# Kernel optimization log

Hardware: AMD Instinct MI355X
Metric: run time of the kernel (lower is better)

Reference implementation:

```python
import jax, jax.numpy as jnp
import numpy as np

N_NODES = 100000
NUM_FEATURES = 64
HIDDEN = 128
OUT_CONV2 = 100


def gcn_conv(x, W, b, src, dst, n):
    """PyG GCNConv: add self-loops, symmetric degree norm, scatter-add."""
    x = x @ W  # [N, out]
    loop = jnp.arange(n, dtype=src.dtype)
    src2 = jnp.concatenate([src, loop])  # [E+N]
    dst2 = jnp.concatenate([dst, loop])
    deg = jax.ops.segment_sum(jnp.ones_like(dst2, dtype=x.dtype), dst2, num_segments=n)
    dinv = jnp.where(deg > 0, deg ** -0.5, 0.0)
    norm = dinv[src2] * dinv[dst2]  # [E+N]
    msg = x[src2] * norm[:, None]  # gather + scale
    out = jax.ops.segment_sum(msg, dst2, num_segments=n)  # scatter-add
    return out + b


def setup_inputs() -> dict:
    key = jax.random.key(0)
    ks = jax.random.split(key, 8)
    E = 1600000
    x = jax.random.normal(ks[0], (N_NODES, NUM_FEATURES), dtype=jnp.float32)
    edge_index = jax.random.randint(ks[1], (2, E), 0, N_NODES, dtype=jnp.int64)
    # Glorot-style init for GCNConv weights, zeros bias (PyG defaults)
    s1 = (6.0 / (NUM_FEATURES + HIDDEN)) ** 0.5
    W1 = jax.random.uniform(ks[2], (NUM_FEATURES, HIDDEN), minval=-s1, maxval=s1, dtype=jnp.float32)
    b1 = jnp.zeros((HIDDEN,), dtype=jnp.float32)
    s2 = (6.0 / (HIDDEN + OUT_CONV2)) ** 0.5
    W2 = jax.random.uniform(ks[3], (HIDDEN, OUT_CONV2), minval=-s2, maxval=s2, dtype=jnp.float32)
    b2 = jnp.zeros((OUT_CONV2,), dtype=jnp.float32)
    sl = (1.0 / OUT_CONV2) ** 0.5
    Wl = jax.random.uniform(ks[4], (OUT_CONV2, 1), minval=-sl, maxval=sl, dtype=jnp.float32)
    bl = jax.random.uniform(ks[5], (1,), minval=-sl, maxval=sl, dtype=jnp.float32)
    return {"x": x, "edge_index": edge_index, "W1": W1, "b1": b1,
            "W2": W2, "b2": b2, "Wl": Wl, "bl": bl}


def reference(x, edge_index, W1, b1, W2, b2, Wl, bl):
    src, dst = edge_index[0], edge_index[1]
    h = gcn_conv(x, W1, b1, src, dst, N_NODES)
    h = jax.nn.relu(h)
    # F.dropout with training=False (eval/inference) is identity
    h = gcn_conv(h, W2, b2, src, dst, N_NODES)
    return h @ Wl + bl  # [N, 1]
```

## Files before the change

kernel.cpp:

```cpp
#include <hip/hip_runtime.h>
#include <hip/hip_fp16.h>


#define N_NODES 100000
#define F_IN 64
#define HID 128
#define OUT2 100
#define BSHIFT 7
#define BNODES 128
#define NBUCKETS ((N_NODES + BNODES - 1) / BNODES)
#define SCAP 2560
#define ACHUNK 4096
#define NB_PAD 1024
#define SENTB 0xFFFFu
#define SENTE 0xFFFFFFFFu
#define TSHIFT 13
#define NTILES 13
#define RSTRIDE 76
#define YSCALE 4096.0f
#define YINV   (1.0f / 4096.0f)
#define ZSCALE 8192.0f
#define ZINV   (1.0f / 8192.0f)

typedef _Float16 half8 __attribute__((ext_vector_type(8)));
typedef float f32x4 __attribute__((ext_vector_type(4)));

static __device__ __forceinline__ half8 as_half8(uint4 u) {
    union { uint4 u; half8 h; } x; x.u = u; return x.h;
}

__global__ __launch_bounds__(256) void prep_kernel(
    const float* __restrict__ W1, const float* __restrict__ W2,
    const float* __restrict__ b2, const float* __restrict__ Wl,
    const float* __restrict__ bl,
    float* __restrict__ v, float* __restrict__ c, uint4* __restrict__ Wpk,
    int* __restrict__ bcur) {
    int t = threadIdx.x;
    if (blockIdx.x < 8) {
        int idx = blockIdx.x * 256 + t;
        int lane2 = idx & 63;
        int kf    = (idx >> 6) & 1;
        int cb    = (idx >> 7) & 7;
        int part  = (idx >> 10) & 1;
        union { uint4 u; unsigned short s[8]; } pk;
        #pragma unroll
        for (int j = 0; j < 8; ++j) {
            int k    = kf * 32 + (lane2 >> 4) * 8 + j;
            int colg = cb * 16 + (lane2 & 15);
            float w = W1[k * HID + colg];
            __half h = __float2half_rn(w);
            if (part) h = __float2half_rn(w - __half2float(h));
            pk.s[j] = __half_as_ushort(h);
        }
        Wpk[idx] = pk.u;
    } else {
        #pragma unroll
        for (int i = 0; i < 4; ++i) bcur[t + i * 256] = (t + i * 256) * SCAP;
        if (t < HID) {
            float acc = 0.f;
            for (int k = 0; k < OUT2; ++k) acc += W2[t * OUT2 + k] * Wl[k];
            v[t] = acc;
        } else if (t == HID) {
            float acc = bl[0];
            for (int k = 0; k < OUT2; ++k) acc += b2[k] * Wl[k];
            *c = acc;
        }
    }
}

__global__ __launch_bounds__(256) void partA_kernel(
    const int* __restrict__ src, const int* __restrict__ dst,
    int* __restrict__ bcur, unsigned int* __restrict__ ebuf, int E) {
    __shared__ unsigned int stage[ACHUNK];
    __shared__ unsigned short sb[ACHUNK];
    __shared__ int hist[NB_PAD];
    __shared__ int ocnt[NB_PAD];
    __shared__ int gbase[NB_PAD];
    __shared__ int cnt2[NB_PAD];
    int t = threadIdx.x;
    int base = blockIdx.x * ACHUNK;
    int total = E - base; if (total > ACHUNK) total = ACHUNK;

    #pragma unroll
    for (int i = 0; i < 4; ++i) { hist[t + i * 256] = 0; cnt2[t + i * 256] = 0; }
    __syncthreads();

    unsigned int pe[16];
    unsigned short bk[16];
    #pragma unroll
    for (int k = 0; k < 16; ++k) {
        int e = base + k * 256 + t;
        if (e < E) {
            int s = src[e], d = dst[e];
            pe[k] = ((unsigned int)s << BSHIFT) | (unsigned int)(d & (BNODES - 1));
            bk[k] = (unsigned short)(d >> BSHIFT);
            atomicAdd(&hist[bk[k]], 1);
        } else {
            bk[k] = SENTB;
        }
    }
    __syncthreads();
    #pragma unroll
    for (int i = 0; i < 4; ++i) ocnt[t + i * 256] = hist[t + i * 256];
    __syncthreads();
    for (int off = 1; off < NB_PAD; off <<= 1) {
        int v4[4];
        #pragma unroll
        for (int i = 0; i < 4; ++i) {
            int p = t + i * 256;
            v4[i] = (p >= off) ? hist[p - off] : 0;
        }
        __syncthreads();
        #pragma unroll
        for (int i = 0; i < 4; ++i) hist[t + i * 256] += v4[i];
        __syncthreads();
    }
    #pragma unroll
    for (int i = 0; i < 4; ++i) {
        int b = (t + i * 256 + blockIdx.x * 131) & (NB_PAD - 1);
        int cc = ocnt[b];
        if (cc > 0 && b < NBUCKETS) gbase[b] = atomicAdd(&bcur[b], cc);
    }
    __syncthreads();
    #pragma unroll
    for (int k = 0; k < 16; ++k) {
        if (bk[k] != SENTB) {
            int b = bk[k];
            int pos = (hist[b] - ocnt[b]) + atomicAdd(&cnt2[b], 1);
            stage[pos] = pe[k];
            sb[pos] = (unsigned short)b;
        }
    }
    __syncthreads();
    #pragma unroll
    for (int k = 0; k < 16; ++k) {
        int idx = k * 256 + t;
        if (idx < total) {
            int b = sb[idx];
            int lo = hist[b] - ocnt[b];
            ebuf[gbase[b] + (idx - lo)] = stage[idx];
        }
    }
}

__global__ __launch_bounds__(256) void partB_kernel(
    const int* __restrict__ bcur, unsigned int* __restrict__ csr,
    float* __restrict__ dinv,
    const float4* __restrict__ x4, uint2* __restrict__ y2, int n) {
    __shared__ int lcnt[BNODES];
    __shared__ float sdinv[BNODES];
    __shared__ int tcnt[16];
    __shared__ int tcur[16];
    __shared__ unsigned int sbuf[SCAP];
    int b = blockIdx.x, t = threadIdx.x;
    int node0 = b << BSHIFT;
    int nlocal = min(BNODES, n - node0);
    int base = b * SCAP;
    int cnt = bcur[b] - base;
    if (t < BNODES) lcnt[t] = 0;
    if (t < 16) tcnt[t] = 0;
    __syncthreads();
    unsigned int er[SCAP / 256];
    #pragma unroll
    for (int k = 0; k < SCAP / 256; ++k) {
        int idx = k * 256 + t;
        er[k] = (idx < cnt) ? csr[base + idx] : SENTE;
        if (er[k] != SENTE) {
            atomicAdd(&lcnt[er[k] & (BNODES - 1)], 1);
            atomicAdd(&tcnt[er[k] >> (BSHIFT + TSHIFT)], 1);
        }
    }
    __syncthreads();
    if (t < BNODES) {
        float sd = rsqrtf((float)lcnt[t] + 1.0f);
        sdinv[t] = sd;
        if (t < nlocal) dinv[node0 + t] = sd;
    }
    if (t == 0) {
        int s = 0;
        #pragma unroll
        for (int i = 0; i < NTILES; ++i) { tcur[i] = s; s += tcnt[i]; }
    }
    __syncthreads();
    #pragma unroll
    for (int k = 0; k < SCAP / 256; ++k) {
        unsigned int e = er[k];
        if (e != SENTE) {
            int p = atomicAdd(&tcur[e >> (BSHIFT + TSHIFT)], 1);
            sbuf[p] = e;
        }
    }
    __syncthreads();
    for (int idx = t; idx < cnt; idx += 256) csr[base + idx] = sbuf[idx];
    for (int i = t; i < nlocal * 16; i += 256) {
        int nl = i >> 4;
        int gi = (node0 + nl) * 16 + (i & 15);
        float sc = sdinv[nl] * YSCALE;
        float4 xv = x4[gi];
        int a0 = __float2int_rn(xv.x * sc);
        int a1 = __float2int_rn(xv.y * sc);
        int a2 = __float2int_rn(xv.z * sc);
        int a3 = __float2int_rn(xv.w * sc);
        uint2 pk;
        pk.x = ((unsigned int)a0 & 0xFFFFu) | ((unsigned int)a1 << 16);
        pk.y = ((unsigned int)a2 & 0xFFFFu) | ((unsigned int)a3 << 16);
        y2[gi] = pk;
    }
}

__global__ __launch_bounds__(256, 4) void fused1_kernel(
    const int4* __restrict__ y4, const short* __restrict__ yh,
    const unsigned int* __restrict__ csr, const int* __restrict__ bcur,
    const float* __restrict__ dinv, const uint4* __restrict__ Wpk,
    const float* __restrict__ b1, const float* __restrict__ v,
    float* __restrict__ zz, int n) {
    __shared__ int acci[BNODES * RSTRIDE];
    int t = threadIdx.x;
    int lane = t & 63, wave = t >> 6;
    int q = lane >> 3, col = lane & 7;
    int b = blockIdx.x;
    int node0 = b << BSHIFT;
    int nlocal = min(BNODES, n - node0);
    int base = b * SCAP;
    int cnt = bcur[b] - base;

    for (int r = wave; r < BNODES; r += 4) {
        int vv = 0;
        if (r < nlocal) vv = (int)yh[(node0 + r) * 64 + lane];
        acci[r * RSTRIDE + (lane >> 3) * 9 + (lane & 7)] = vv;
    }
    __syncthreads();

    int nr = (cnt + 255) >> 8;
    int p0 = wave * 64 + lane;
    unsigned int ee = (p0 < cnt) ? csr[base + p0] : SENTE;
    for (int r = 0; r < nr; ++r) {
        int pn = (r + 1) * 256 + wave * 64 + lane;
        unsigned int ee_n = (pn < cnt) ? csr[base + pn] : SENTE;
        int4 u[8];
        int dl[8];
        #pragma unroll
        for (int g = 0; g < 8; ++g) {
            unsigned int e = __shfl(ee, g * 8 + q, 64);
            bool valid = (e != SENTE);
            int srow = valid ? (int)(e >> BSHIFT) : 0;
            dl[g] = (int)(e & (BNODES - 1));
            u[g] = y4[srow * 8 + col];
            if (!valid) u[g] = (int4){0, 0, 0, 0};
        }
        #pragma unroll
        for (int g = 0; g < 8; ++g) {
            int* rowp = &acci[dl[g] * RSTRIDE + col * 9];
            const int* up = (const int*)&u[g];
            #pragma unroll
            for (int j = 0; j < 4; ++j) {
                int d = up[j];
                atomicAdd(&rowp[2 * j],     (d << 16) >> 16);
                atomicAdd(&rowp[2 * j + 1], d >> 16);
            }
        }
        ee = ee_n;
    }
    __syncthreads();

    int mm = lane & 15, kq = lane >> 4;
    for (int i = 0; i < 2; ++i) {
        int st = wave * 2 + i;
        int row = st * 16 + mm;
        float dis = ((row < nlocal) ? dinv[node0 + row] : 0.f) * YINV;
        const int* ap = &acci[row * RSTRIDE];
        half8 A0, A1;
        #pragma unroll
        for (int j = 0; j < 8; ++j) {
            A0[j] = (_Float16)(dis * (float)ap[kq * 9 + j]);
            A1[j] = (_Float16)(dis * (float)ap[(4 + kq) * 9 + j]);
        }
        f32x4 acc[8];
        #pragma unroll
        for (int cb = 0; cb < 8; ++cb) acc[cb] = (f32x4){0.f, 0.f, 0.f, 0.f};
        #pragma unroll
        for (int cb = 0; cb < 8; ++cb) {
            half8 bh0 = as_half8(Wpk[(cb * 2 + 0) * 64 + lane]);
            half8 bh1 = as_half8(Wpk[(cb * 2 + 1) * 64 + lane]);
            half8 bl0 = as_half8(Wpk[1024 + (cb * 2 + 0) * 64 + lane]);
            half8 bl1 = as_half8(Wpk[1024 + (cb * 2 + 1) * 64 + lane]);
            acc[cb] = __builtin_amdgcn_mfma_f32_16x16x32_f16(A0, bh0, acc[cb], 0, 0, 0);
            acc[cb] = __builtin_amdgcn_mfma_f32_16x16x32_f16(A1, bh1, acc[cb], 0, 0, 0);
            acc[cb] = __builtin_amdgcn_mfma_f32_16x16x32_f16(A0, bl0, acc[cb], 0, 0, 0);
            acc[cb] = __builtin_amdgcn_mfma_f32_16x16x32_f16(A1, bl1, acc[cb], 0, 0, 0);
        }
        float zp[4] = {0.f, 0.f, 0.f, 0.f};
        #pragma unroll
        for (int cb = 0; cb < 8; ++cb) {
            int colg = cb * 16 + mm;
            float bb1 = b1[colg], vv = v[colg];
            #pragma unroll
            for (int rr = 0; rr < 4; ++rr) {
                float h = acc[cb][rr] + bb1;
                h = fmaxf(h, 0.f);
                zp[rr] += h * vv;
            }
        }
        #pragma unroll
        for (int off = 1; off < 16; off <<= 1) {
            #pragma unroll
            for (int rr = 0; rr < 4; ++rr) zp[rr] += __shfl_xor(zp[rr], off, 64);
        }
        if (mm == 0) {
            int nb = st * 16 + kq * 4;
            #pragma unroll
            for (int rr = 0; rr < 4; ++rr)
                if (nb + rr < nlocal)
                    zz[node0 + nb + rr] = dinv[node0 + nb + rr] * zp[rr];
        }
    }
}

__global__ __launch_bounds__(256) void out_kernel(
    const int* __restrict__ bcur, const unsigned int* __restrict__ csr,
    const float* __restrict__ dinv, const float* __restrict__ zz,
    const float* __restrict__ c, float* __restrict__ out, int n) {
    __shared__ int acc2[BNODES];
    int b = blockIdx.x, t = threadIdx.x;
    int node0 = b << BSHIFT;
    int nlocal = min(BNODES, n - node0);
    int base = b * SCAP;
    int cnt = bcur[b] - base;
    if (t < BNODES) acc2[t] = 0;
    __syncthreads();
    for (int idx = t; idx < cnt; idx += 256) {
        unsigned int e = csr[base + idx];
        float z = zz[e >> BSHIFT];
        atomicAdd(&acc2[e & (BNODES - 1)], __float2int_rn(z * ZSCALE));
    }
    __syncthreads();
    if (t < nlocal) {
        int node = node0 + t;
        out[node] = c[0] + dinv[node] * ((float)acc2[t] * ZINV + zz[node]);
    }
}

extern "C" void kernel_launch(void* const* d_in, const int* in_sizes, int n_in,
                              void* d_out, int out_size, void* d_ws, size_t ws_size,
                              hipStream_t stream) {
    const float* x  = (const float*)d_in[0];
    const int*   ei = (const int*)d_in[1];
    const float* W1 = (const float*)d_in[2];
    const float* b1 = (const float*)d_in[3];
    const float* W2 = (const float*)d_in[4];
    const float* b2 = (const float*)d_in[5];
    const float* Wl = (const float*)d_in[6];
    const float* bl = (const float*)d_in[7];
    float* out = (float*)d_out;

    int E = in_sizes[1] / 2;
    const int* src = ei;
    const int* dst = ei + E;

    float* ws      = (float*)d_ws;
    float* dinv    = ws;
    float* zz      = dinv + N_NODES;
    float* v       = zz + N_NODES;
    float* c       = v + HID;
    int*   bcur    = (int*)(c + 4);
    int*   csr     = bcur + NB_PAD;
    uint4* Wpk     = (uint4*)(csr + (size_t)NBUCKETS * SCAP);
    short* y       = (short*)((float*)Wpk + 8192);

    int nchunks = (E + ACHUNK - 1) / ACHUNK;

    prep_kernel<<<9, 256, 0, stream>>>(W1, W2, b2, Wl, bl, v, c, Wpk, bcur);
    partA_kernel<<<nchunks, 256, 0, stream>>>(src, dst, bcur, (unsigned int*)csr, E);
    partB_kernel<<<NBUCKETS, 256, 0, stream>>>(
        bcur, (unsigned int*)csr, dinv, (const float4*)x, (uint2*)y, N_NODES);
    fused1_kernel<<<NBUCKETS, 256, 0, stream>>>(
        (const int4*)y, (const short*)y, (const unsigned int*)csr,
        bcur, dinv, Wpk, b1, v, zz, N_NODES);
    out_kernel<<<NBUCKETS, 256, 0, stream>>>(
        bcur, (const unsigned int*)csr, dinv, zz, c, out, N_NODES);
}
```

Baseline: 178.0 us.

## Replace two-pass edge partitioning with atomic binning by bucket and source tile

The shared-memory histogram, prefix-scan partition kernel is replaced by a scatter kernel. It takes one global atomic per edge on fixed-capacity bins keyed by destination bucket and source tile. A compact kernel then packs each bucket's bins into a tile-sorted CSR, computes degrees, and writes the quantized features into the same buffer region it has just read. The fused aggregation loop now prefetches edge data and gathers two rounds ahead, and the shared accumulator row stride changes. This removes a scan and several barriers, but it relies on no bin exceeding 256 edges and adds global atomic contention.

```diff
diff --git a/kernel.cpp b/kernel.cpp
--- a/kernel.cpp
+++ b/kernel.cpp
@@ -11,12 +11,12 @@
 #define NBUCKETS ((N_NODES + BNODES - 1) / BNODES)
 #define SCAP 2560
 #define ACHUNK 4096
-#define NB_PAD 1024
-#define SENTB 0xFFFFu
 #define SENTE 0xFFFFFFFFu
 #define TSHIFT 13
 #define NTILES 13
-#define RSTRIDE 76
+#define TCAP 256
+#define NBINS (NBUCKETS * 16)
+#define RSTRIDE 77
 #define YSCALE 4096.0f
 #define YINV   (1.0f / 4096.0f)
 #define ZSCALE 8192.0f
@@ -34,7 +34,7 @@
     const float* __restrict__ b2, const float* __restrict__ Wl,
     const float* __restrict__ bl,
     float* __restrict__ v, float* __restrict__ c, uint4* __restrict__ Wpk,
-    int* __restrict__ bcur) {
+    int* __restrict__ bcur2) {
     int t = threadIdx.x;
     if (blockIdx.x < 8) {
         int idx = blockIdx.x * 256 + t;
@@ -54,8 +54,7 @@
         }
         Wpk[idx] = pk.u;
     } else {
-        #pragma unroll
-        for (int i = 0; i < 4; ++i) bcur[t + i * 256] = (t + i * 256) * SCAP;
+        for (int i = t; i < NBINS; i += 256) bcur2[i] = i << 8;
         if (t < HID) {
             float acc = 0.f;
             for (int k = 0; k < OUT2; ++k) acc += W2[t * OUT2 + k] * Wl[k];
@@ -68,108 +67,46 @@
     }
 }
 
-__global__ __launch_bounds__(256) void partA_kernel(
+__global__ __launch_bounds__(256) void scatter_kernel(
     const int* __restrict__ src, const int* __restrict__ dst,
-    int* __restrict__ bcur, unsigned int* __restrict__ ebuf, int E) {
-    __shared__ unsigned int stage[ACHUNK];
-    __shared__ unsigned short sb[ACHUNK];
-    __shared__ int hist[NB_PAD];
-    __shared__ int ocnt[NB_PAD];
-    __shared__ int gbase[NB_PAD];
-    __shared__ int cnt2[NB_PAD];
+    int* __restrict__ bcur2, int* __restrict__ buf, int E) {
     int t = threadIdx.x;
     int base = blockIdx.x * ACHUNK;
-    int total = E - base; if (total > ACHUNK) total = ACHUNK;
-
-    #pragma unroll
-    for (int i = 0; i < 4; ++i) { hist[t + i * 256] = 0; cnt2[t + i * 256] = 0; }
-    __syncthreads();
-
-    unsigned int pe[16];
-    unsigned short bk[16];
     #pragma unroll
     for (int k = 0; k < 16; ++k) {
         int e = base + k * 256 + t;
         if (e < E) {
             int s = src[e], d = dst[e];
-            pe[k] = ((unsigned int)s << BSHIFT) | (unsigned int)(d & (BNODES - 1));
-            bk[k] = (unsigned short)(d >> BSHIFT);
-            atomicAdd(&hist[bk[k]], 1);
-        } else {
-            bk[k] = SENTB;
-        }
-    }
-    __syncthreads();
-    #pragma unroll
-    for (int i = 0; i < 4; ++i) ocnt[t + i * 256] = hist[t + i * 256];
-    __syncthreads();
-    for (int off = 1; off < NB_PAD; off <<= 1) {
-        int v4[4];
-        #pragma unroll
-        for (int i = 0; i < 4; ++i) {
-            int p = t + i * 256;
-            v4[i] = (p >= off) ? hist[p - off] : 0;
-        }
-        __syncthreads();
-        #pragma unroll
-        for (int i = 0; i < 4; ++i) hist[t + i * 256] += v4[i];
-        __syncthreads();
-    }
-    #pragma unroll
-    for (int i = 0; i < 4; ++i) {
-        int b = (t + i * 256 + blockIdx.x * 131) & (NB_PAD - 1);
-        int cc = ocnt[b];
-        if (cc > 0 && b < NBUCKETS) gbase[b] = atomicAdd(&bcur[b], cc);
-    }
-    __syncthreads();
-    #pragma unroll
-    for (int k = 0; k < 16; ++k) {
-        if (bk[k] != SENTB) {
-            int b = bk[k];
-            int pos = (hist[b] - ocnt[b]) + atomicAdd(&cnt2[b], 1);
-            stage[pos] = pe[k];
-            sb[pos] = (unsigned short)b;
-        }
-    }
-    __syncthreads();
-    #pragma unroll
-    for (int k = 0; k < 16; ++k) {
-        int idx = k * 256 + t;
-        if (idx < total) {
-            int b = sb[idx];
-            int lo = hist[b] - ocnt[b];
-            ebuf[gbase[b] + (idx - lo)] = stage[idx];
-        }
-    }
-}
-
-__global__ __launch_bounds__(256) void partB_kernel(
-    const int* __restrict__ bcur, unsigned int* __restrict__ csr,
-    float* __restrict__ dinv,
-    const float4* __restrict__ x4, uint2* __restrict__ y2, int n) {
+            int bin = ((d >> BSHIFT) << 4) | (s >> TSHIFT);
+            int pos = atomicAdd(&bcur2[bin], 1);
+            buf[pos] = (s << BSHIFT) | (d & (BNODES - 1));
+        }
+    }
+}
+
+__global__ __launch_bounds__(256) void compact_kernel(
+    const int* __restrict__ bcur2, int* __restrict__ buf,
+    unsigned int* __restrict__ csrP, int* __restrict__ bcnt,
+    float* __restrict__ dinv, const float4* __restrict__ x4, int n) {
+    __shared__ int scnt[16];
+    __shared__ int soff[16];
     __shared__ int lcnt[BNODES];
     __shared__ float sdinv[BNODES];
-    __shared__ int tcnt[16];
-    __shared__ int tcur[16];
-    __shared__ unsigned int sbuf[SCAP];
     int b = blockIdx.x, t = threadIdx.x;
     int node0 = b << BSHIFT;
     int nlocal = min(BNODES, n - node0);
-    int base = b * SCAP;
-    int cnt = bcur[b] - base;
+    int binbase = b << 12;
+    if (t < 16) scnt[t] = bcur2[(b << 4) | t] - (((b << 4) | t) << 8);
     if (t < BNODES) lcnt[t] = 0;
-    if (t < 16) tcnt[t] = 0;
-    __syncthreads();
-    unsigned int er[SCAP / 256];
-    #pragma unroll
-    for (int k = 0; k < SCAP / 256; ++k) {
-        int idx = k * 256 + t;
-        er[k] = (idx < cnt) ? csr[base + idx] : SENTE;
-        if (er[k] != SENTE) {
-            atomicAdd(&lcnt[er[k] & (BNODES - 1)], 1);
-            atomicAdd(&tcnt[er[k] >> (BSHIFT + TSHIFT)], 1);
-        }
-    }
+    __syncthreads();
+    int er[16];
+    #pragma unroll
+    for (int i = 0; i < 16; ++i) er[i] = buf[binbase + (i << 8) + t];
+    #pragma unroll
+    for (int i = 0; i < NTILES; ++i)
+        if (t < scnt[i]) atomicAdd(&lcnt[er[i] & (BNODES - 1)], 1);
+    #pragma unroll
+    for (int i = 0; i < 16; ++i) asm volatile("" :: "v"(er[i]));
     __syncthreads();
     if (t < BNODES) {
         float sd = rsqrtf((float)lcnt[t] + 1.0f);
@@ -179,19 +116,14 @@
     if (t == 0) {
         int s = 0;
         #pragma unroll
-        for (int i = 0; i < NTILES; ++i) { tcur[i] = s; s += tcnt[i]; }
-    }
-    __syncthreads();
-    #pragma unroll
-    for (int k = 0; k < SCAP / 256; ++k) {
-        unsigned int e = er[k];
-        if (e != SENTE) {
-            int p = atomicAdd(&tcur[e >> (BSHIFT + TSHIFT)], 1);
-            sbuf[p] = e;
-        }
-    }
-    __syncthreads();
-    for (int idx = t; idx < cnt; idx += 256) csr[base + idx] = sbuf[idx];
+        for (int i = 0; i < NTILES; ++i) {
+            soff[i] = s;
+            s += min(scnt[i], TCAP);
+        }
+        soff[NTILES] = s;
+    }
+    __syncthreads();
+    uint2* y2 = (uint2*)buf;
     for (int i = t; i < nlocal * 16; i += 256) {
         int nl = i >> 4;
         int gi = (node0 + nl) * 16 + (i & 15);
@@ -206,11 +138,40 @@
         pk.y = ((unsigned int)a2 & 0xFFFFu) | ((unsigned int)a3 << 16);
         y2[gi] = pk;
     }
-}
+    int base2 = b * SCAP;
+    #pragma unroll
+    for (int i = 0; i < NTILES; ++i)
+        if (t < scnt[i]) csrP[base2 + soff[i] + t] = (unsigned int)er[i];
+    if (t == 0) bcnt[b] = soff[NTILES];
+}
+
+#define F1_ISSUE(EE, U, DL)                                            \
+    _Pragma("unroll")                                                  \
+    for (int g = 0; g < 8; ++g) {                                      \
+        unsigned int e_ = __shfl((EE), g * 8 + q, 64);                 \
+        bool valid_ = (e_ != SENTE);                                   \
+        int srow_ = valid_ ? (int)(e_ >> BSHIFT) : 0;                  \
+        DL[g] = (int)(e_ & (BNODES - 1));                              \
+        U[g] = y4[srow_ * 8 + col];                                    \
+        if (!valid_) U[g] = (int4){0, 0, 0, 0};                        \
+    }
+
+#define F1_CONSUME(U, DL)                                              \
+    _Pragma("unroll")                                                  \
+    for (int g = 0; g < 8; ++g) {                                      \
+        int* rowp_ = &acci[DL[g] * RSTRIDE + col * 9];                 \
+        const int* up_ = (const int*)&U[g];                            \
+        _Pragma("unroll")                                              \
+        for (int j = 0; j < 4; ++j) {                                  \
+            int d_ = up_[j];                                           \
+            atomicAdd(&rowp_[2 * j],     (d_ << 16) >> 16);            \
+            atomicAdd(&rowp_[2 * j + 1], d_ >> 16);                    \
+        }                                                              \
+    }
 
 __global__ __launch_bounds__(256, 4) void fused1_kernel(
     const int4* __restrict__ y4, const short* __restrict__ yh,
-    const unsigned int* __restrict__ csr, const int* __restrict__ bcur,
+    const unsigned int* __restrict__ csrP, const int* __restrict__ bcnt,
     const float* __restrict__ dinv, const uint4* __restrict__ Wpk,
     const float* __restrict__ b1, const float* __restrict__ v,
     float* __restrict__ zz, int n) {
@@ -222,7 +183,7 @@
     int node0 = b << BSHIFT;
     int nlocal = min(BNODES, n - node0);
     int base = b * SCAP;
-    int cnt = bcur[b] - base;
+    int cnt = bcnt[b];
 
     for (int r = wave; r < BNODES; r += 4) {
         int vv = 0;
@@ -232,34 +193,20 @@
     __syncthreads();
 
     int nr = (cnt + 255) >> 8;
-    int p0 = wave * 64 + lane;
-    unsigned int ee = (p0 < cnt) ? csr[base + p0] : SENTE;
+    int lpos = wave * 64 + lane;
+    unsigned int eeA = (lpos < cnt) ? csrP[base + lpos] : SENTE;
+    int4 uA[8]; int dlA[8];
+    F1_ISSUE(eeA, uA, dlA);
+    unsigned int eeB = (lpos + 256 < cnt) ? csrP[base + lpos + 256] : SENTE;
+    #pragma unroll 2
     for (int r = 0; r < nr; ++r) {
-        int pn = (r + 1) * 256 + wave * 64 + lane;
-        unsigned int ee_n = (pn < cnt) ? csr[base + pn] : SENTE;
-        int4 u[8];
-        int dl[8];
-        #pragma unroll
-        for (int g = 0; g < 8; ++g) {
-            unsigned int e = __shfl(ee, g * 8 + q, 64);
-            bool valid = (e != SENTE);
-            int srow = valid ? (int)(e >> BSHIFT) : 0;
-            dl[g] = (int)(e & (BNODES - 1));
-            u[g] = y4[srow * 8 + col];
-            if (!valid) u[g] = (int4){0, 0, 0, 0};
-        }
-        #pragma unroll
-        for (int g = 0; g < 8; ++g) {
-            int* rowp = &acci[dl[g] * RSTRIDE + col * 9];
-            const int* up = (const int*)&u[g];
-            #pragma unroll
-            for (int j = 0; j < 4; ++j) {
-                int d = up[j];
-                atomicAdd(&rowp[2 * j],     (d << 16) >> 16);
-                atomicAdd(&rowp[2 * j + 1], d >> 16);
-            }
-        }
-        ee = ee_n;
+        int4 uN[8]; int dlN[8];
+        F1_ISSUE(eeB, uN, dlN);
+        int pn = lpos + (r + 2) * 256;
+        eeB = (pn < cnt) ? csrP[base + pn] : SENTE;
+        F1_CONSUME(uA, dlA);
+        #pragma unroll
+        for (int g = 0; g < 8; ++g) { uA[g] = uN[g]; dlA[g] = dlN[g]; }
     }
     __syncthreads();
 
@@ -317,7 +264,7 @@
 }
 
 __global__ __launch_bounds__(256) void out_kernel(
-    const int* __restrict__ bcur, const unsigned int* __restrict__ csr,
+    const int* __restrict__ bcnt, const unsigned int* __restrict__ csrP,
     const float* __restrict__ dinv, const float* __restrict__ zz,
     const float* __restrict__ c, float* __restrict__ out, int n) {
     __shared__ int acc2[BNODES];
@@ -325,11 +272,11 @@
     int node0 = b << BSHIFT;
     int nlocal = min(BNODES, n - node0);
     int base = b * SCAP;
-    int cnt = bcur[b] - base;
+    int cnt = bcnt[b];
     if (t < BNODES) acc2[t] = 0;
     __syncthreads();
     for (int idx = t; idx < cnt; idx += 256) {
-        unsigned int e = csr[base + idx];
+        unsigned int e = csrP[base + idx];
         float z = zz[e >> BSHIFT];
         atomicAdd(&acc2[e & (BNODES - 1)], __float2int_rn(z * ZSCALE));
     }
@@ -362,20 +309,21 @@
     float* zz      = dinv + N_NODES;
     float* v       = zz + N_NODES;
     float* c       = v + HID;
-    int*   bcur    = (int*)(c + 4);
-    int*   csr     = bcur + NB_PAD;
-    uint4* Wpk     = (uint4*)(csr + (size_t)NBUCKETS * SCAP);
-    short* y       = (short*)((float*)Wpk + 8192);
+    int*   bcur2   = (int*)(c + 4);
+    int*   bcnt    = bcur2 + NBINS;
+    int*   csrP    = bcnt + 784;
+    uint4* Wpk     = (uint4*)(csrP + (size_t)NBUCKETS * SCAP);
+    int*   buf     = (int*)((float*)Wpk + 8192);
 
     int nchunks = (E + ACHUNK - 1) / ACHUNK;
 
-    prep_kernel<<<9, 256, 0, stream>>>(W1, W2, b2, Wl, bl, v, c, Wpk, bcur);
-    partA_kernel<<<nchunks, 256, 0, stream>>>(src, dst, bcur, (unsigned int*)csr, E);
-    partB_kernel<<<NBUCKETS, 256, 0, stream>>>(
-        bcur, (unsigned int*)csr, dinv, (const float4*)x, (uint2*)y, N_NODES);
+    prep_kernel<<<9, 256, 0, stream>>>(W1, W2, b2, Wl, bl, v, c, Wpk, bcur2);
+    scatter_kernel<<<nchunks, 256, 0, stream>>>(src, dst, bcur2, buf, E);
+    compact_kernel<<<NBUCKETS, 256, 0, stream>>>(
+        bcur2, buf, (unsigned int*)csrP, bcnt, dinv, (const float4*)x, N_NODES);
     fused1_kernel<<<NBUCKETS, 256, 0, stream>>>(
-        (const int4*)y, (const short*)y, (const unsigned int*)csr,
-        bcur, dinv, Wpk, b1, v, zz, N_NODES);
+        (const int4*)buf, (const short*)buf, (const unsigned int*)csrP,
+        bcnt, dinv, Wpk, b1, v, zz, N_NODES);
     out_kernel<<<NBUCKETS, 256, 0, stream>>>(
-        bcur, (const unsigned int*)csr, dinv, zz, c, out, N_NODES);
-}
+        bcnt, (const unsigned int*)csrP, dinv, zz, c, out, N_NODES);
+}
```

Measured after the change: 244.1 us. +37.2%, slower.

## Merge prep into partitioning kernel and software-pipeline fused1 gather loop

Applied to the files above, without the earlier changes.

Folds the weight-prep work into extra blocks of the edge-partition kernel and replaces the bucket cursor initialisation with a memset storing relative counts. This removes one kernel launch and its serialisation. The fused1 edge loop now issues the next round's gathers before the current round's shared-memory atomics, using a zeroed sentinel row instead of per-element masking. The LDS row stride changes from 76 to 77 to reduce bank conflicts. The deeper pipeline raises register pressure, which may hurt occupancy under the 4-block launch bound.

```diff
diff --git a/kernel.cpp b/kernel.cpp
--- a/kernel.cpp
+++ b/kernel.cpp
@@ -16,7 +16,8 @@
 #define SENTE 0xFFFFFFFFu
 #define TSHIFT 13
 #define NTILES 13
-#define RSTRIDE 76
+#define RSTRIDE 77
+#define ZROW N_NODES
 #define YSCALE 4096.0f
 #define YINV   (1.0f / 4096.0f)
 #define ZSCALE 8192.0f
@@ -29,55 +30,54 @@
     union { uint4 u; half8 h; } x; x.u = u; return x.h;
 }
 
-__global__ __launch_bounds__(256) void prep_kernel(
+__global__ __launch_bounds__(256) void partA_kernel(
+    const int* __restrict__ src, const int* __restrict__ dst,
+    int* __restrict__ bcur, unsigned int* __restrict__ ebuf, int E, int nchunks,
     const float* __restrict__ W1, const float* __restrict__ W2,
     const float* __restrict__ b2, const float* __restrict__ Wl,
     const float* __restrict__ bl,
     float* __restrict__ v, float* __restrict__ c, uint4* __restrict__ Wpk,
-    int* __restrict__ bcur) {
+    int* __restrict__ yzero) {
     int t = threadIdx.x;
-    if (blockIdx.x < 8) {
-        int idx = blockIdx.x * 256 + t;
-        int lane2 = idx & 63;
-        int kf    = (idx >> 6) & 1;
-        int cb    = (idx >> 7) & 7;
-        int part  = (idx >> 10) & 1;
-        union { uint4 u; unsigned short s[8]; } pk;
-        #pragma unroll
-        for (int j = 0; j < 8; ++j) {
-            int k    = kf * 32 + (lane2 >> 4) * 8 + j;
-            int colg = cb * 16 + (lane2 & 15);
-            float w = W1[k * HID + colg];
-            __half h = __float2half_rn(w);
-            if (part) h = __float2half_rn(w - __half2float(h));
-            pk.s[j] = __half_as_ushort(h);
-        }
-        Wpk[idx] = pk.u;
-    } else {
-        #pragma unroll
-        for (int i = 0; i < 4; ++i) bcur[t + i * 256] = (t + i * 256) * SCAP;
-        if (t < HID) {
-            float acc = 0.f;
-            for (int k = 0; k < OUT2; ++k) acc += W2[t * OUT2 + k] * Wl[k];
-            v[t] = acc;
-        } else if (t == HID) {
-            float acc = bl[0];
-            for (int k = 0; k < OUT2; ++k) acc += b2[k] * Wl[k];
-            *c = acc;
-        }
-    }
-}
-
-__global__ __launch_bounds__(256) void partA_kernel(
-    const int* __restrict__ src, const int* __restrict__ dst,
-    int* __restrict__ bcur, unsigned int* __restrict__ ebuf, int E) {
+    if ((int)blockIdx.x >= nchunks) {
+        int pb = (int)blockIdx.x - nchunks;
+        if (pb < 8) {
+            int idx = pb * 256 + t;
+            int lane2 = idx & 63;
+            int kf    = (idx >> 6) & 1;
+            int cb    = (idx >> 7) & 7;
+            int part  = (idx >> 10) & 1;
+            union { uint4 u; unsigned short s[8]; } pk;
+            #pragma unroll
+            for (int j = 0; j < 8; ++j) {
+                int k    = kf * 32 + (lane2 >> 4) * 8 + j;
+                int colg = cb * 16 + (lane2 & 15);
+                float w = W1[k * HID + colg];
+                __half h = __float2half_rn(w);
+                if (part) h = __float2half_rn(w - __half2float(h));
+                pk.s[j] = __half_as_ushort(h);
+            }
+            Wpk[idx] = pk.u;
+        } else {
+            if (t < HID) {
+                float acc = 0.f;
+                for (int k = 0; k < OUT2; ++k) acc += W2[t * OUT2 + k] * Wl[k];
+                v[t] = acc;
+            } else if (t == HID) {
+                float acc = bl[0];
+                for (int k = 0; k < OUT2; ++k) acc += b2[k] * Wl[k];
+                *c = acc;
+            }
+            if (t < 128) yzero[t] = 0;
+        }
+        return;
+    }
     __shared__ unsigned int stage[ACHUNK];
     __shared__ unsigned short sb[ACHUNK];
     __shared__ int hist[NB_PAD];
     __shared__ int ocnt[NB_PAD];
     __shared__ int gbase[NB_PAD];
     __shared__ int cnt2[NB_PAD];
-    int t = threadIdx.x;
     int base = blockIdx.x * ACHUNK;
     int total = E - base; if (total > ACHUNK) total = ACHUNK;
 
@@ -119,7 +119,8 @@
     for (int i = 0; i < 4; ++i) {
         int b = (t + i * 256 + blockIdx.x * 131) & (NB_PAD - 1);
         int cc = ocnt[b];
-        if (cc > 0 && b < NBUCKETS) gbase[b] = atomicAdd(&bcur[b], cc);
+        if (cc > 0 && b < NBUCKETS)
+            gbase[b] = b * SCAP + atomicAdd(&bcur[b], cc);
     }
     __syncthreads();
     #pragma unroll
@@ -156,7 +157,7 @@
     int node0 = b << BSHIFT;
     int nlocal = min(BNODES, n - node0);
     int base = b * SCAP;
-    int cnt = bcur[b] - base;
+    int cnt = bcur[b];
     if (t < BNODES) lcnt[t] = 0;
     if (t < 16) tcnt[t] = 0;
     __syncthreads();
@@ -208,6 +209,28 @@
     }
 }
 
+#define F1_ISSUE(EE, U, DL)                                            \
+    _Pragma("unroll")                                                  \
+    for (int g = 0; g < 8; ++g) {                                      \
+        unsigned int e_ = __shfl((EE), g * 8 + q, 64);                 \
+        int srow_ = (e_ != SENTE) ? (int)(e_ >> BSHIFT) : ZROW;        \
+        DL[g] = (int)(e_ & (BNODES - 1));                              \
+        U[g] = y4[srow_ * 8 + col];                                    \
+    }
+
+#define F1_CONSUME(U, DL)                                              \
+    _Pragma("unroll")                                                  \
+    for (int g = 0; g < 8; ++g) {                                      \
+        int* rowp_ = &acci[DL[g] * RSTRIDE + col * 9];                 \
+        const int* up_ = (const int*)&U[g];                            \
+        _Pragma("unroll")                                              \
+        for (int j = 0; j < 4; ++j) {                                  \
+            int d_ = up_[j];                                           \
+            atomicAdd(&rowp_[2 * j],     (d_ << 16) >> 16);            \
+            atomicAdd(&rowp_[2 * j + 1], d_ >> 16);                    \
+        }                                                              \
+    }
+
 __global__ __launch_bounds__(256, 4) void fused1_kernel(
     const int4* __restrict__ y4, const short* __restrict__ yh,
     const unsigned int* __restrict__ csr, const int* __restrict__ bcur,
@@ -222,7 +245,7 @@
     int node0 = b << BSHIFT;
     int nlocal = min(BNODES, n - node0);
     int base = b * SCAP;
-    int cnt = bcur[b] - base;
+    int cnt = bcur[b];
 
     for (int r = wave; r < BNODES; r += 4) {
         int vv = 0;
@@ -232,34 +255,20 @@
     __syncthreads();
 
     int nr = (cnt + 255) >> 8;
-    int p0 = wave * 64 + lane;
-    unsigned int ee = (p0 < cnt) ? csr[base + p0] : SENTE;
+    int lpos = wave * 64 + lane;
+    unsigned int eeA = (lpos < cnt) ? csr[base + lpos] : SENTE;
+    int4 uA[8]; int dlA[8];
+    F1_ISSUE(eeA, uA, dlA);
+    unsigned int eeB = (lpos + 256 < cnt) ? csr[base + lpos + 256] : SENTE;
+    #pragma unroll 2
     for (int r = 0; r < nr; ++r) {
-        int pn = (r + 1) * 256 + wave * 64 + lane;
-        unsigned int ee_n = (pn < cnt) ? csr[base + pn] : SENTE;
-        int4 u[8];
-        int dl[8];
-        #pragma unroll
-        for (int g = 0; g < 8; ++g) {
-            unsigned int e = __shfl(ee, g * 8 + q, 64);
-            bool valid = (e != SENTE);
-            int srow = valid ? (int)(e >> BSHIFT) : 0;
-            dl[g] = (int)(e & (BNODES - 1));
-            u[g] = y4[srow * 8 + col];
-            if (!valid) u[g] = (int4){0, 0, 0, 0};
-        }
-        #pragma unroll
-        for (int g = 0; g < 8; ++g) {
-            int* rowp = &acci[dl[g] * RSTRIDE + col * 9];
-            const int* up = (const int*)&u[g];
-            #pragma unroll
-            for (int j = 0; j < 4; ++j) {
-                int d = up[j];
-                atomicAdd(&rowp[2 * j],     (d << 16) >> 16);
-                atomicAdd(&rowp[2 * j + 1], d >> 16);
-            }
-        }
-        ee = ee_n;
+        int4 uN[8]; int dlN[8];
+        F1_ISSUE(eeB, uN, dlN);
+        int pn = lpos + (r + 2) * 256;
+        eeB = (pn < cnt) ? csr[base + pn] : SENTE;
+        F1_CONSUME(uA, dlA);
+        #pragma unroll
+        for (int g = 0; g < 8; ++g) { uA[g] = uN[g]; dlA[g] = dlN[g]; }
     }
     __syncthreads();
 
@@ -325,7 +334,7 @@
     int node0 = b << BSHIFT;
     int nlocal = min(BNODES, n - node0);
     int base = b * SCAP;
-    int cnt = bcur[b] - base;
+    int cnt = bcur[b];
     if (t < BNODES) acc2[t] = 0;
     __syncthreads();
     for (int idx = t; idx < cnt; idx += 256) {
@@ -369,8 +378,10 @@
 
     int nchunks = (E + ACHUNK - 1) / ACHUNK;
 
-    prep_kernel<<<9, 256, 0, stream>>>(W1, W2, b2, Wl, bl, v, c, Wpk, bcur);
-    partA_kernel<<<nchunks, 256, 0, stream>>>(src, dst, bcur, (unsigned int*)csr, E);
+    hipMemsetAsync(bcur, 0, NBUCKETS * sizeof(int), stream);
+    partA_kernel<<<nchunks + 9, 256, 0, stream>>>(
+        src, dst, bcur, (unsigned int*)csr, E, nchunks,
+        W1, W2, b2, Wl, bl, v, c, Wpk, (int*)(y + (size_t)ZROW * 64));
     partB_kernel<<<NBUCKETS, 256, 0, stream>>>(
         bcur, (unsigned int*)csr, dinv, (const float4*)x, (uint2*)y, N_NODES);
     fused1_kernel<<<NBUCKETS, 256, 0, stream>>>(
```

After: 182.4 us. +2.5%, slower.
